# Performance work log

Hardware: AMD Instinct MI355X
Metric: run time of the kernel (lower is better)

## Reference

```python
import jax, jax.numpy as jnp
import numpy as np

B, H, W, C = 2, 64, 64, 256
NH, K = 8, 7  # num_heads, neighborhood kernel size


def setup_inputs() -> dict:
    key = jax.random.key(0)
    ks = jax.random.split(key, 8)
    xav = lambda k, shape: jax.random.normal(k, shape, jnp.float32) * np.sqrt(2.0 / (shape[0] + shape[1])).astype(np.float32)
    return {
        "x": jax.random.normal(ks[0], (B, H, W, C), jnp.float32),
        "norm1_g": jnp.ones((C,), jnp.float32),
        "norm1_b": jnp.zeros((C,), jnp.float32),
        "qkv_w": xav(ks[1], (3 * C, C)),
        "qkv_b": jnp.zeros((3 * C,), jnp.float32),
        "rpb": jax.random.normal(ks[2], (NH, 2 * K - 1, 2 * K - 1), jnp.float32) * 0.02,
        "proj_w": xav(ks[3], (C, C)),
        "proj_b": jnp.zeros((C,), jnp.float32),
        "norm2_g": jnp.ones((C,), jnp.float32),
        "norm2_b": jnp.zeros((C,), jnp.float32),
        "fc1_w": xav(ks[4], (4 * C, C)),
        "fc1_b": jnp.zeros((4 * C,), jnp.float32),
        "fc2_w": xav(ks[5], (C, 4 * C)),
        "fc2_b": jnp.zeros((C,), jnp.float32),
    }


def _layernorm(x, g, b, eps=1e-5):
    m = x.mean(-1, keepdims=True)
    v = jnp.mean((x - m) ** 2, axis=-1, keepdims=True)
    return (x - m) * jax.lax.rsqrt(v + eps) * g + b


def _nat2d(x, qkv_w, qkv_b, rpb, proj_w, proj_b):
    """Neighborhood attention 2D (NATTEN semantics: edge-clamped k x k windows,
    relative positional bias indexed by key_pos - query_pos + k - 1)."""
    b, h, w, c = x.shape
    nh = rpb.shape[0]
    k = (rpb.shape[1] + 1) // 2
    dh = c // nh
    qkv = (x @ qkv_w.T + qkv_b).reshape(b, h, w, 3, nh, dh)
    q = qkv[..., 0, :, :] * (dh ** -0.5)  # [b,h,w,nh,dh]
    kk = qkv[..., 1, :, :]
    vv = qkv[..., 2, :, :]
    # edge-clamped window starts per query row/col
    starts_h = jnp.clip(jnp.arange(h) - k // 2, 0, h - k)
    starts_w = jnp.clip(jnp.arange(w) - k // 2, 0, w - k)
    idx_h = starts_h[:, None] + jnp.arange(k)  # [h,k] key row indices
    idx_w = starts_w[:, None] + jnp.arange(k)  # [w,k] key col indices
    # gather neighborhoods -> [b,h,w,k,k,nh,dh]
    knb = kk[:, idx_h][:, :, :, idx_w].transpose(0, 1, 3, 2, 4, 5, 6)
    vnb = vv[:, idx_h][:, :, :, idx_w].transpose(0, 1, 3, 2, 4, 5, 6)
    attn = jnp.einsum('bijhd,bijklhd->bijhkl', q, knb)  # [b,h,w,nh,k,k]
    # relative positional bias: index = key - query + (k-1) in [0, 2k-2]
    rb_h = idx_h - jnp.arange(h)[:, None] + (k - 1)  # [h,k]
    rb_w = idx_w - jnp.arange(w)[:, None] + (k - 1)  # [w,k]
    bias = rpb[:, rb_h][:, :, :, rb_w]  # [nh,h,k,w,k]
    bias = bias.transpose(1, 3, 0, 2, 4)  # [h,w,nh,k,k]
    attn = jax.nn.softmax((attn + bias).reshape(b, h, w, nh, k * k), axis=-1)
    out = jnp.einsum('bijhn,bijnhd->bijhd', attn, vnb.reshape(b, h, w, k * k, nh, dh))
    return out.reshape(b, h, w, c) @ proj_w.T + proj_b


def reference(x, norm1_g, norm1_b, qkv_w, qkv_b, rpb, proj_w, proj_b,
              norm2_g, norm2_b, fc1_w, fc1_b, fc2_w, fc2_b):
    # norm -> neighborhood attention -> residual
    x = x + _nat2d(_layernorm(x, norm1_g, norm1_b), qkv_w, qkv_b, rpb, proj_w, proj_b)
    # norm -> MLP (gelu) -> residual
    hdn = _layernorm(x, norm2_g, norm2_b)
    hdn = jax.nn.gelu(hdn @ fc1_w.T + fc1_b, approximate=False)
    return x + (hdn @ fc2_w.T + fc2_b)
```

## Files before the change

### kernel.cpp

```cpp
#include <hip/hip_runtime.h>

typedef __attribute__((ext_vector_type(8))) short bf16x8;
typedef __attribute__((ext_vector_type(4))) float f32x4;
typedef unsigned short u16;

__device__ __forceinline__ float bf2f(u16 u) {
    return __builtin_bit_cast(float, ((unsigned int)u) << 16);
}
__device__ __forceinline__ u16 f2bf(float f) {
    unsigned int x = __builtin_bit_cast(unsigned int, f);
    x += 0x7FFFu + ((x >> 16) & 1u);
    return (u16)(x >> 16);
}

typedef const __attribute__((address_space(1))) void* gas_t;
typedef __attribute__((address_space(3))) void* las_t;
__device__ __forceinline__ void load_lds16(const u16* g, u16* l) {
    __builtin_amdgcn_global_load_lds((gas_t)g, (las_t)l, 16, 0, 0);
}

__global__ __launch_bounds__(256) void cvt_kernel(
    const float* __restrict__ s0, const float* __restrict__ s1,
    const float* __restrict__ s2, const float* __restrict__ s3,
    u16* __restrict__ dst)
{
    const int i4 = (blockIdx.x * 256 + threadIdx.x) * 4;
    const float* src;
    int off;
    if      (i4 < 196608) { src = s0; off = i4; }
    else if (i4 < 262144) { src = s1; off = i4 - 196608; }
    else if (i4 < 524288) { src = s2; off = i4 - 262144; }
    else                  { src = s3; off = i4 - 524288; }
    float4 v = *(const float4*)(src + off);
    ushort4 o;
    o.x = f2bf(v.x); o.y = f2bf(v.y); o.z = f2bf(v.z); o.w = f2bf(v.w);
    *(ushort4*)(dst + i4) = o;
}

__global__ __launch_bounds__(256) void ln_kernel(
    const float* __restrict__ x, const float* __restrict__ g,
    const float* __restrict__ b, u16* __restrict__ y)
{
    const int tok  = blockIdx.x * 4 + (threadIdx.x >> 6);
    const int lane = threadIdx.x & 63;
    float4 v = *(const float4*)(x + (size_t)tok * 256 + lane * 4);
    float s  = v.x + v.y + v.z + v.w;
    float sq = v.x*v.x + v.y*v.y + v.z*v.z + v.w*v.w;
    #pragma unroll
    for (int off = 32; off; off >>= 1) {
        s  += __shfl_xor(s, off);
        sq += __shfl_xor(sq, off);
    }
    float mean = s * (1.0f / 256.0f);
    float var  = sq * (1.0f / 256.0f) - mean * mean;
    float rs   = rsqrtf(var + 1e-5f);
    float4 gv = *(const float4*)(g + lane * 4);
    float4 bv = *(const float4*)(b + lane * 4);
    ushort4 o;
    o.x = f2bf((v.x - mean) * rs * gv.x + bv.x);
    o.y = f2bf((v.y - mean) * rs * gv.y + bv.y);
    o.z = f2bf((v.z - mean) * rs * gv.z + bv.z);
    o.w = f2bf((v.w - mean) * rs * gv.w + bv.w);
    *(ushort4*)(y + (size_t)tok * 256 + lane * 4) = o;
}

template<int BN, int N, int K, int EPI>
__global__ __launch_bounds__(256) void gemm_lds(
    const u16* __restrict__ A, const u16* __restrict__ W,
    const float* __restrict__ bias, const float* __restrict__ res,
    void* __restrict__ outv)
{
    constexpr int NT = BN / 32;
    __shared__ u16 As[128 * 32];
    __shared__ u16 Bs[BN * 32];
    const int tid  = threadIdx.x;
    const int lane = tid & 63;
    const int wave = tid >> 6;
    const int m0   = blockIdx.x * 128;
    const int n0   = blockIdx.y * BN;
    const int wmb  = (wave >> 1) * 64;
    const int wnb  = (wave & 1) * (BN / 2);

    f32x4 acc[4][NT];
    #pragma unroll
    for (int mt = 0; mt < 4; ++mt)
        #pragma unroll
        for (int nt = 0; nt < NT; ++nt)
            acc[mt][nt] = (f32x4){0.f, 0.f, 0.f, 0.f};

    const int srow = tid >> 2;
    const int skc  = (tid & 3) * 8;
    const int fr   = lane & 15;
    const int fk   = (lane >> 4) * 8;

    for (int k0 = 0; k0 < K; k0 += 32) {
        __syncthreads();
        load_lds16(A + (size_t)(m0 + srow) * K + k0 + skc,      As + tid * 8);
        load_lds16(A + (size_t)(m0 + 64 + srow) * K + k0 + skc, As + 2048 + tid * 8);
        load_lds16(W + (size_t)(n0 + srow) * K + k0 + skc,      Bs + tid * 8);
        if (BN == 128)
            load_lds16(W + (size_t)(n0 + 64 + srow) * K + k0 + skc, Bs + 2048 + tid * 8);
        __syncthreads();
        bf16x8 af[4], bf[NT];
        #pragma unroll
        for (int mt = 0; mt < 4; ++mt)
            af[mt] = *(const bf16x8*)(As + (wmb + mt * 16 + fr) * 32 + fk);
        #pragma unroll
        for (int nt = 0; nt < NT; ++nt)
            bf[nt] = *(const bf16x8*)(Bs + (wnb + nt * 16 + fr) * 32 + fk);
        #pragma unroll
        for (int mt = 0; mt < 4; ++mt)
            #pragma unroll
            for (int nt = 0; nt < NT; ++nt)
                acc[mt][nt] = __builtin_amdgcn_mfma_f32_16x16x32_bf16(af[mt], bf[nt], acc[mt][nt], 0, 0, 0);
    }

    const int col = lane & 15;
    const int rb  = (lane >> 4) * 4;
    #pragma unroll
    for (int nt = 0; nt < NT; ++nt) {
        const int n  = n0 + wnb + nt * 16 + col;
        const float bv = bias[n];
        #pragma unroll
        for (int mt = 0; mt < 4; ++mt) {
            #pragma unroll
            for (int r = 0; r < 4; ++r) {
                const int m = m0 + wmb + mt * 16 + rb + r;
                float v = acc[mt][nt][r] + bv;
                if (EPI == 1) {
                    if (n < 256) v *= 0.1767766952966369f;
                    ((u16*)outv)[(size_t)m * N + n] = f2bf(v);
                }
                if (EPI == 2) {
                    v += res[(size_t)m * N + n];
                    ((float*)outv)[(size_t)m * N + n] = v;
                }
                if (EPI == 3) {
                    v = 0.5f * v * (1.0f + erff(v * 0.7071067811865475f));
                    ((u16*)outv)[(size_t)m * N + n] = f2bf(v);
                }
            }
        }
    }
}

__global__ __launch_bounds__(256, 2) void attn_tile_kernel(
    const u16* __restrict__ qkv, const float* __restrict__ rpb,
    u16* __restrict__ out)
{
    __shared__ u16   kv[100 * 64];
    __shared__ u16   qs[16 * 32];
    __shared__ float probs[16 * 66];

    const int tid  = threadIdx.x;
    const int bb   = blockIdx.x >> 8;
    const int rem  = blockIdx.x & 255;
    const int ti0  = (rem >> 4) << 2;
    const int tj0  = (rem & 15) << 2;
    const int oh   = min(max(ti0 - 3, 0), 54);
    const int ow   = min(max(tj0 - 3, 0), 54);
    const int tokbase = bb * 4096;

    int off_kv[4];
    #pragma unroll
    for (int r = 0; r < 4; ++r) {
        const int s  = r * 256 + tid;
        const int t  = s >> 3;
        const int cs = s & 7;
        const int c  = cs ^ (t & 7);
        const int tr = t / 10, tc = t - tr * 10;
        const int tokg = tokbase + (oh + tr) * 64 + (ow + tc);
        off_kv[r] = tokg * 768 + 256 + ((c & 4) << 6) + (c & 3) * 8;
    }
    const int tq   = tid >> 2;
    const int qoff = (tokbase + (ti0 + (tq >> 2)) * 64 + (tj0 + (tq & 3))) * 768
                   + (tid & 3) * 8;

    const int token = tid >> 4;
    const int part  = tid & 15;
    const int li = token >> 2, lj = token & 3;
    const int i  = ti0 + li,   j  = tj0 + lj;
    const int sh = min(max(i - 3, 0), 57);
    const int sw = min(max(j - 3, 0), 57);
    const int rowbase  = (sh - oh) * 10 + (sw - ow);
    const int rb_const = (sh - i + 6) * 13 + (sw - j + 6);
    const size_t outbase = (size_t)(tokbase + i * 64 + j) * 256 + part * 2;

    for (int h = 0; h < 8; ++h) {
        __syncthreads();
        const int hoff = h * 32;
        #pragma unroll
        for (int r = 0; r < 3; ++r)
            load_lds16(qkv + off_kv[r] + hoff, kv + (r * 256 + tid) * 8);
        if (tid < 32)
            load_lds16(qkv + off_kv[3] + hoff, kv + (768 + tid) * 8);
        if (tid < 64)
            load_lds16(qkv + qoff + hoff, qs + tid * 8);
        __syncthreads();

        float qv[32];
        #pragma unroll
        for (int c = 0; c < 4; ++c) {
            bf16x8 v = *(const bf16x8*)(qs + token * 32 + c * 8);
            #pragma unroll
            for (int e = 0; e < 8; ++e) qv[c * 8 + e] = bf2f((u16)v[e]);
        }

        float sc[4];
        #pragma unroll
        for (int sidx = 0; sidx < 4; ++sidx) {
            const int n = part + sidx * 16;
            if (n < 49) {
                const int kh = n / 7, kw = n - (n / 7) * 7;
                const int hidx = rowbase + kh * 10 + kw;
                float acc = rpb[h * 169 + rb_const + kh * 13 + kw];
                #pragma unroll
                for (int c = 0; c < 4; ++c) {
                    const int slot = (hidx << 3) + (c ^ (hidx & 7));
                    bf16x8 kk = *(const bf16x8*)(kv + slot * 8);
                    #pragma unroll
                    for (int e = 0; e < 8; ++e)
                        acc += qv[c * 8 + e] * bf2f((u16)kk[e]);
                }
                sc[sidx] = acc;
            } else {
                sc[sidx] = -1e30f;
            }
        }
        float mx = fmaxf(fmaxf(sc[0], sc[1]), fmaxf(sc[2], sc[3]));
        #pragma unroll
        for (int off = 1; off < 16; off <<= 1) mx = fmaxf(mx, __shfl_xor(mx, off));
        float ex[4], ssum = 0.f;
        #pragma unroll
        for (int sidx = 0; sidx < 4; ++sidx) {
            ex[sidx] = __expf(sc[sidx] - mx);
            ssum += ex[sidx];
        }
        #pragma unroll
        for (int off = 1; off < 16; off <<= 1) ssum += __shfl_xor(ssum, off);
        const float inv = 1.0f / ssum;
        #pragma unroll
        for (int sidx = 0; sidx < 4; ++sidx)
            probs[token * 66 + part + sidx * 16] = ex[sidx] * inv;
        __syncthreads();

        float o0 = 0.f, o1 = 0.f;
        const int vchunk = 4 + (part >> 2);
        const int vsub   = (part & 3) * 2;
        #pragma unroll
        for (int kh = 0; kh < 7; ++kh) {
            #pragma unroll
            for (int kw = 0; kw < 7; ++kw) {
                const int n    = kh * 7 + kw;
                const int hidx = rowbase + kh * 10 + kw;
                const float p  = probs[token * 66 + n];
                const int slot = (hidx << 3) + (vchunk ^ (hidx & 7));
                const unsigned int vv = *(const unsigned int*)(kv + slot * 8 + vsub);
                o0 += p * bf2f((u16)(vv & 0xffffu));
                o1 += p * bf2f((u16)(vv >> 16));
            }
        }
        ushort2 ov;
        ov.x = f2bf(o0); ov.y = f2bf(o1);
        *(ushort2*)(out + outbase + hoff) = ov;
    }
}

extern "C" void kernel_launch(void* const* d_in, const int* in_sizes, int n_in,
                              void* d_out, int out_size, void* d_ws, size_t ws_size,
                              hipStream_t stream)
{
    const float* x      = (const float*)d_in[0];
    const float* n1g    = (const float*)d_in[1];
    const float* n1b    = (const float*)d_in[2];
    const float* qkv_w  = (const float*)d_in[3];
    const float* qkv_b  = (const float*)d_in[4];
    const float* rpb    = (const float*)d_in[5];
    const float* proj_w = (const float*)d_in[6];
    const float* proj_b = (const float*)d_in[7];
    const float* n2g    = (const float*)d_in[8];
    const float* n2b    = (const float*)d_in[9];
    const float* fc1_w  = (const float*)d_in[10];
    const float* fc1_b  = (const float*)d_in[11];
    const float* fc2_w  = (const float*)d_in[12];
    const float* fc2_b  = (const float*)d_in[13];
    float* out = (float*)d_out;

    char* wsb = (char*)d_ws;
    u16*   wbf   = (u16*)wsb;
    u16*   qkvW  = wbf;
    u16*   projW = wbf + 196608;
    u16*   fc1W  = wbf + 262144;
    u16*   fc2W  = wbf + 524288;
    u16*   ln1   = (u16*)(wsb + 1572864);
    u16*   attn  = ln1;
    u16*   qkvB  = (u16*)(wsb + 5767168);
    u16*   ln2   = qkvB;
    u16*   hbuf  = (u16*)(wsb + 9961472);
    float* x1    = (float*)(wsb + 26738688);

    dim3 blk(256);
    cvt_kernel<<<768, blk, 0, stream>>>(qkv_w, proj_w, fc1_w, fc2_w, wbf);
    ln_kernel<<<2048, blk, 0, stream>>>(x, n1g, n1b, ln1);
    gemm_lds<128, 768, 256, 1><<<dim3(64, 6), blk, 0, stream>>>(ln1, qkvW, qkv_b, nullptr, qkvB);
    attn_tile_kernel<<<512, blk, 0, stream>>>(qkvB, rpb, attn);
    gemm_lds<64, 256, 256, 2><<<dim3(64, 4), blk, 0, stream>>>(attn, projW, proj_b, x, x1);
    ln_kernel<<<2048, blk, 0, stream>>>(x1, n2g, n2b, ln2);
    gemm_lds<128, 1024, 256, 3><<<dim3(64, 8), blk, 0, stream>>>(ln2, fc1W, fc1_b, nullptr, hbuf);
    gemm_lds<64, 256, 1024, 2><<<dim3(64, 4), blk, 0, stream>>>(hbuf, fc2W, fc2_b, x1, out);
}
```

Before: 174.6 us.

## Replace GEMM with 64x64 tiles, BK=64, and XOR-swizzled LDS layout

All four GEMMs now use a single 64x64 output tile kernel with a K-step of 64 and an XOR swizzle on the LDS chunk index, which avoids bank conflicts on the fragment reads. Smaller tiles launch 2-4x more blocks, filling the many CUs on MI355X better. Larger K-steps halve the number of sync iterations. The trade-off is less data reuse per block and more global traffic from reloading A and W tiles.

```diff
diff --git a/kernel.cpp b/kernel.cpp
--- a/kernel.cpp
+++ b/kernel.cpp
@@ -64,68 +64,82 @@
     *(ushort4*)(y + (size_t)tok * 256 + lane * 4) = o;
 }
 
-template<int BN, int N, int K, int EPI>
-__global__ __launch_bounds__(256) void gemm_lds(
+template<int N, int K, int EPI>
+__global__ __launch_bounds__(256) void gemm64(
     const u16* __restrict__ A, const u16* __restrict__ W,
     const float* __restrict__ bias, const float* __restrict__ res,
     void* __restrict__ outv)
 {
-    constexpr int NT = BN / 32;
-    __shared__ u16 As[128 * 32];
-    __shared__ u16 Bs[BN * 32];
+    __shared__ u16 As[64 * 64];
+    __shared__ u16 Bs[64 * 64];
     const int tid  = threadIdx.x;
     const int lane = tid & 63;
     const int wave = tid >> 6;
-    const int m0   = blockIdx.x * 128;
-    const int n0   = blockIdx.y * BN;
-    const int wmb  = (wave >> 1) * 64;
-    const int wnb  = (wave & 1) * (BN / 2);
-
-    f32x4 acc[4][NT];
-    #pragma unroll
-    for (int mt = 0; mt < 4; ++mt)
-        #pragma unroll
-        for (int nt = 0; nt < NT; ++nt)
+    const int m0   = blockIdx.x * 64;
+    const int n0   = blockIdx.y * 64;
+    const int wm0  = (wave >> 1) * 32;
+    const int wn0  = (wave & 1) * 32;
+
+    f32x4 acc[2][2];
+    #pragma unroll
+    for (int mt = 0; mt < 2; ++mt)
+        #pragma unroll
+        for (int nt = 0; nt < 2; ++nt)
             acc[mt][nt] = (f32x4){0.f, 0.f, 0.f, 0.f};
 
-    const int srow = tid >> 2;
-    const int skc  = (tid & 3) * 8;
-    const int fr   = lane & 15;
-    const int fk   = (lane >> 4) * 8;
-
-    for (int k0 = 0; k0 < K; k0 += 32) {
-        __syncthreads();
-        load_lds16(A + (size_t)(m0 + srow) * K + k0 + skc,      As + tid * 8);
-        load_lds16(A + (size_t)(m0 + 64 + srow) * K + k0 + skc, As + 2048 + tid * 8);
-        load_lds16(W + (size_t)(n0 + srow) * K + k0 + skc,      Bs + tid * 8);
-        if (BN == 128)
-            load_lds16(W + (size_t)(n0 + 64 + srow) * K + k0 + skc, Bs + 2048 + tid * 8);
-        __syncthreads();
-        bf16x8 af[4], bf[NT];
-        #pragma unroll
-        for (int mt = 0; mt < 4; ++mt)
-            af[mt] = *(const bf16x8*)(As + (wmb + mt * 16 + fr) * 32 + fk);
-        #pragma unroll
-        for (int nt = 0; nt < NT; ++nt)
-            bf[nt] = *(const bf16x8*)(Bs + (wnb + nt * 16 + fr) * 32 + fk);
-        #pragma unroll
-        for (int mt = 0; mt < 4; ++mt)
-            #pragma unroll
-            for (int nt = 0; nt < NT; ++nt)
-                acc[mt][nt] = __builtin_amdgcn_mfma_f32_16x16x32_bf16(af[mt], bf[nt], acc[mt][nt], 0, 0, 0);
+    int soff[2];
+    #pragma unroll
+    for (int r = 0; r < 2; ++r) {
+        const int s   = r * 256 + tid;
+        const int row = s >> 3;
+        const int c   = (s & 7) ^ (row & 7);
+        soff[r] = row * K + c * 8;
+    }
+    const int fr = lane & 15;
+    const int fc = lane >> 4;
+
+    for (int k0 = 0; k0 < K; k0 += 64) {
+        __syncthreads();
+        #pragma unroll
+        for (int r = 0; r < 2; ++r) {
+            load_lds16(A + (size_t)m0 * K + k0 + soff[r], As + (r * 256 + tid) * 8);
+            load_lds16(W + (size_t)n0 * K + k0 + soff[r], Bs + (r * 256 + tid) * 8);
+        }
+        __syncthreads();
+        #pragma unroll
+        for (int ks = 0; ks < 2; ++ks) {
+            bf16x8 af[2], bw[2];
+            #pragma unroll
+            for (int mt = 0; mt < 2; ++mt) {
+                const int rr   = wm0 + mt * 16 + fr;
+                const int phys = (ks * 4 + fc) ^ (rr & 7);
+                af[mt] = *(const bf16x8*)(As + rr * 64 + phys * 8);
+            }
+            #pragma unroll
+            for (int nt = 0; nt < 2; ++nt) {
+                const int rr   = wn0 + nt * 16 + fr;
+                const int phys = (ks * 4 + fc) ^ (rr & 7);
+                bw[nt] = *(const bf16x8*)(Bs + rr * 64 + phys * 8);
+            }
+            #pragma unroll
+            for (int mt = 0; mt < 2; ++mt)
+                #pragma unroll
+                for (int nt = 0; nt < 2; ++nt)
+                    acc[mt][nt] = __builtin_amdgcn_mfma_f32_16x16x32_bf16(af[mt], bw[nt], acc[mt][nt], 0, 0, 0);
+        }
     }
 
     const int col = lane & 15;
     const int rb  = (lane >> 4) * 4;
     #pragma unroll
-    for (int nt = 0; nt < NT; ++nt) {
-        const int n  = n0 + wnb + nt * 16 + col;
+    for (int nt = 0; nt < 2; ++nt) {
+        const int n  = n0 + wn0 + nt * 16 + col;
         const float bv = bias[n];
         #pragma unroll
-        for (int mt = 0; mt < 4; ++mt) {
+        for (int mt = 0; mt < 2; ++mt) {
             #pragma unroll
             for (int r = 0; r < 4; ++r) {
-                const int m = m0 + wmb + mt * 16 + rb + r;
+                const int m = m0 + wm0 + mt * 16 + rb + r;
                 float v = acc[mt][nt][r] + bv;
                 if (EPI == 1) {
                     if (n < 256) v *= 0.1767766952966369f;
@@ -302,10 +316,10 @@
     dim3 blk(256);
     cvt_kernel<<<768, blk, 0, stream>>>(qkv_w, proj_w, fc1_w, fc2_w, wbf);
     ln_kernel<<<2048, blk, 0, stream>>>(x, n1g, n1b, ln1);
-    gemm_lds<128, 768, 256, 1><<<dim3(64, 6), blk, 0, stream>>>(ln1, qkvW, qkv_b, nullptr, qkvB);
+    gemm64<768, 256, 1><<<dim3(128, 12), blk, 0, stream>>>(ln1, qkvW, qkv_b, nullptr, qkvB);
     attn_tile_kernel<<<512, blk, 0, stream>>>(qkvB, rpb, attn);
-    gemm_lds<64, 256, 256, 2><<<dim3(64, 4), blk, 0, stream>>>(attn, projW, proj_b, x, x1);
+    gemm64<256, 256, 2><<<dim3(128, 4), blk, 0, stream>>>(attn, projW, proj_b, x, x1);
     ln_kernel<<<2048, blk, 0, stream>>>(x1, n2g, n2b, ln2);
-    gemm_lds<128, 1024, 256, 3><<<dim3(64, 8), blk, 0, stream>>>(ln2, fc1W, fc1_b, nullptr, hbuf);
-    gemm_lds<64, 256, 1024, 2><<<dim3(64, 4), blk, 0, stream>>>(hbuf, fc2W, fc2_b, x1, out);
-}
+    gemm64<1024, 256, 3><<<dim3(128, 16), blk, 0, stream>>>(ln2, fc1W, fc1_b, nullptr, hbuf);
+    gemm64<256, 1024, 2><<<dim3(128, 4), blk, 0, stream>>>(hbuf, fc2W, fc2_b, x1, out);
+}
```

After: 165.1 us. 5.5% less time.
